# Optimization experiments

Hardware: AMD Instinct MI355X
Metric: run time of the kernel (lower is better)

Reference implementation:

```python
import jax, jax.numpy as jnp
import numpy as np

N_NODES = 100000


def _segment_mean(h, src, dst, n_nodes):
    # copy_u: gather source features along edges, then mean-reduce per dst node
    msg = h[src]                                             # [E, D]
    s = jax.ops.segment_sum(msg, dst, num_segments=n_nodes)  # [N, D]
    cnt = jax.ops.segment_sum(jnp.ones((src.shape[0],), h.dtype), dst,
                              num_segments=n_nodes)          # [N]
    return s / jnp.maximum(cnt, 1.0)[:, None]


def setup_inputs() -> dict:
    key = jax.random.key(0)
    k1, k2, k3, k4, k5 = jax.random.split(key, 5)
    in_feats, n_hidden, n_classes = 128, 128, 64
    n_edges = 1600000
    features = jax.random.normal(k1, (N_NODES, in_feats), dtype=jnp.float32)
    W1 = jax.random.normal(k2, (in_feats, n_hidden), dtype=jnp.float32) * (1.0 / np.sqrt(in_feats))
    b1 = jnp.zeros((n_hidden,), jnp.float32)
    W2 = jax.random.normal(k3, (n_hidden, n_classes), dtype=jnp.float32) * (1.0 / np.sqrt(n_hidden))
    b2 = jnp.zeros((n_classes,), jnp.float32)
    src = jax.random.randint(k4, (n_edges,), 0, N_NODES, dtype=jnp.int64)
    dst = jax.random.randint(k5, (n_edges,), 0, N_NODES, dtype=jnp.int64)
    return {"features": features, "W1": W1, "b1": b1, "W2": W2, "b2": b2,
            "src": src, "dst": dst}


def reference(features, W1, b1, W2, b2, src, dst):
    # Layer 0: mean aggregation -> Linear -> relu  (dropout p=0.0 is identity)
    h = _segment_mean(features, src, dst, N_NODES)
    h = jax.nn.relu(h @ W1 + b1)
    # Layer 1: mean aggregation -> Linear (no activation on output layer)
    h = _segment_mean(h, src, dst, N_NODES)
    h = h @ W2 + b2
    return h
```

## Files before the change

kernel.cpp:

```cpp
#include <hip/hip_runtime.h>

#define N_NODES 100000
#define D 128
#define NE 1600000
#define C_OUT 64
#define NB 391
#define SENT 100000
#define P2B 320
#define P2E 5000
#define SEGSTRIDE 5120

typedef _Float16 half8 __attribute__((ext_vector_type(8)));
typedef float floatx4 __attribute__((ext_vector_type(4)));


__device__ inline half8 shfl_xor_h8(half8 v, int mask) {
    union { half8 h; int i[4]; } u;
    u.h = v;
    u.i[0] = __shfl_xor(u.i[0], mask);
    u.i[1] = __shfl_xor(u.i[1], mask);
    u.i[2] = __shfl_xor(u.i[2], mask);
    u.i[3] = __shfl_xor(u.i[3], mask);
    return u.h;
}

__device__ inline void pack_one(const float* W, _Float16* Wp, int tid, int N) {
    int l = tid & 63, p = tid >> 6;
    int nt = p >> 2, kc = p & 3;
    int quad = l >> 4, c = l & 15;
    int n = nt * 16 + c;
    half8 h;
    #pragma unroll
    for (int j = 0; j < 8; ++j) {
        int k = kc * 32 + quad * 8 + j;
        h[j] = (_Float16)W[k * N + n];
    }
    *(half8*)(Wp + (size_t)p * 512 + l * 8) = h;
}

__global__ __launch_bounds__(256) void setup_kernel(const float* __restrict__ W1,
                                                    const float* __restrict__ W2,
                                                    _Float16* __restrict__ wp1,
                                                    _Float16* __restrict__ wp2,
                                                    int* __restrict__ t1s,
                                                    int* __restrict__ t2s) {
    const int blk = blockIdx.x;
    const int t = threadIdx.x;
    if (blk < 8) {
        pack_one(W1, wp1, blk * 256 + t, 128);
    } else if (blk < 12) {
        pack_one(W2, wp2, (blk - 8) * 256 + t, 64);
    } else {
        if (t < 64) t1s[t] = 0;
        else if (t < 96) t2s[t - 64] = 0;
    }
}

__global__ __launch_bounds__(1024) void p2_part(const int* __restrict__ src,
                                                const int* __restrict__ dst,
                                                unsigned* __restrict__ gwords,
                                                int* __restrict__ ofsg) {
    __shared__ unsigned ebuf[P2E];
    __shared__ int hist[NB];
    __shared__ int ofs[NB + 1];
    __shared__ int cur[NB];
    __shared__ int sc[512];
    const int t = threadIdx.x;
    const int base = blockIdx.x * P2E;

    for (int i = t; i < NB; i += 1024) hist[i] = 0;
    __syncthreads();

    unsigned w[5];
    int bk[5];
    #pragma unroll
    for (int r = 0; r < 5; ++r) {
        const int e = base + r * 1024 + t;
        if (r * 1024 + t < P2E) {
            const int d = dst[e];
            w[r] = ((unsigned)(d & 255) << 20) | (unsigned)src[e];
            bk[r] = d >> 8;
            atomicAdd(&hist[bk[r]], 1);
        } else {
            bk[r] = -1;
        }
    }
    __syncthreads();

    if (t < 512) sc[t] = (t < NB) ? hist[t] : 0;
    __syncthreads();
    for (int off = 1; off < 512; off <<= 1) {
        int y = 0;
        if (t < 512 && t >= off) y = sc[t - off];
        __syncthreads();
        if (t < 512) sc[t] += y;
        __syncthreads();
    }
    if (t < NB) {
        const int ex = sc[t] - hist[t];
        ofs[t] = ex;
        cur[t] = ex;
    }
    if (t == 0) ofs[NB] = P2E;
    __syncthreads();

    #pragma unroll
    for (int r = 0; r < 5; ++r) {
        if (bk[r] >= 0) {
            const int slot = atomicAdd(&cur[bk[r]], 1);
            ebuf[slot] = w[r];
        }
    }
    __syncthreads();

    unsigned* gout = gwords + (size_t)blockIdx.x * SEGSTRIDE;
    for (int i = t; i < P2E; i += 1024) gout[i] = ebuf[i];
    int* oout = ofsg + blockIdx.x * (NB + 1);
    for (int i = t; i < NB + 1; i += 1024) oout[i] = ofs[i];
}

__global__ __launch_bounds__(512) void p_scan2(const int* __restrict__ ofsg,
                                               int* __restrict__ bbase) {
    __shared__ int lds[512];
    const int t = threadIdx.x;
    int tot = 0;
    if (t < NB) {
        for (int blk = 0; blk < P2B; ++blk) {
            const int* row = ofsg + blk * (NB + 1);
            tot += row[t + 1] - row[t];
        }
    }
    lds[t] = tot;
    __syncthreads();
    for (int off = 1; off < 512; off <<= 1) {
        int y = (t >= off) ? lds[t - off] : 0;
        __syncthreads();
        lds[t] += y;
        __syncthreads();
    }
    if (t < NB) bbase[t] = lds[t] - tot;
    if (t == 0) bbase[NB] = NE;
}

__global__ __launch_bounds__(256) void p3_finalize(const unsigned* __restrict__ gwords,
                                                   const int* __restrict__ ofsg,
                                                   const int* __restrict__ bbase,
                                                   int* __restrict__ ptrp,
                                                   int* __restrict__ pcnt,
                                                   float* __restrict__ inv,
                                                   int* __restrict__ csr) {
    __shared__ unsigned wbuf[8192];
    __shared__ int lcnt[256];
    __shared__ int lofs[256];
    __shared__ int cursor;
    const int b = blockIdx.x;
    const int t = threadIdx.x;
    if (t == 0) cursor = 0;
    lcnt[t] = 0;
    __syncthreads();

    for (int blk = t; blk < P2B; blk += 256) {
        const int* row = ofsg + blk * (NB + 1);
        const int a = row[b];
        const int len = row[b + 1] - a;
        if (len > 0) {
            const int o = atomicAdd(&cursor, len);
            if (o + len <= 8192) {
                const unsigned* s = gwords + (size_t)blk * SEGSTRIDE + a;
                for (int j = 0; j < len; ++j) {
                    const unsigned w = s[j];
                    wbuf[o + j] = w;
                    atomicAdd(&lcnt[(w >> 20) & 255], 1);
                }
            }
        }
    }
    __syncthreads();

    const int tot = cursor;
    const int v = lcnt[t];
    const int pc = (v + 7) & ~7;
    lofs[t] = pc;
    __syncthreads();
    for (int off = 1; off < 256; off <<= 1) {
        int y = (t >= off) ? lofs[t - off] : 0;
        __syncthreads();
        lofs[t] += y;
        __syncthreads();
    }
    const int ex = lofs[t] - pc;
    const int pad_base = bbase[b] + 1792 * b;

    const int node = b * 256 + t;
    if (node < N_NODES) {
        ptrp[node] = pad_base + ex;
        pcnt[node] = pc;
        inv[node] = 1.0f / fmaxf((float)v, 1.0f);
    }
    for (int j = v; j < pc; ++j) csr[pad_base + ex + j] = SENT;

    __syncthreads();
    lofs[t] = ex;
    __syncthreads();
    for (int i = t; i < tot; i += 256) {
        const unsigned w = wbuf[i];
        const int pos = atomicAdd(&lofs[(w >> 20) & 255], 1);
        csr[pad_base + pos] = (int)(w & 0xFFFFF);
    }
}

__global__ __launch_bounds__(256) void gemm1(const float* __restrict__ A,
                                             const _Float16* __restrict__ Wp,
                                             _Float16* __restrict__ outh) {
    __shared__ __align__(16) _Float16 Wl[16384];
    __shared__ __align__(16) _Float16 Al[4096];
    const int t = threadIdx.x;
    {
        const floatx4* s4 = (const floatx4*)Wp;
        floatx4* d4 = (floatx4*)Wl;
        #pragma unroll
        for (int i = 0; i < 8; ++i) d4[t + 256 * i] = s4[t + 256 * i];
    }
    const int lane = t & 63;
    const int wave = t >> 6;
    const int row0 = blockIdx.x * 128;

    floatx4 acc[8][2];
    #pragma unroll
    for (int mt = 0; mt < 8; ++mt)
        #pragma unroll
        for (int nt = 0; nt < 2; ++nt) acc[mt][nt] = (floatx4)0.0f;

    for (int kc = 0; kc < 4; ++kc) {
        __syncthreads();
        #pragma unroll
        for (int rep = 0; rep < 2; ++rep) {
            int p = rep * 256 + t;
            int r = p >> 2, quad = p & 3;
            int row = row0 + r;
            if (row > N_NODES - 1) row = N_NODES - 1;
            const float4 x0 = *(const float4*)(A + (size_t)row * D + kc * 32 + quad * 8);
            const float4 x1 = *(const float4*)(A + (size_t)row * D + kc * 32 + quad * 8 + 4);
            half8 h;
            h[0] = (_Float16)x0.x; h[1] = (_Float16)x0.y;
            h[2] = (_Float16)x0.z; h[3] = (_Float16)x0.w;
            h[4] = (_Float16)x1.x; h[5] = (_Float16)x1.y;
            h[6] = (_Float16)x1.z; h[7] = (_Float16)x1.w;
            int mt = r >> 4, m = r & 15;
            *(half8*)(Al + mt * 512 + (quad * 16 + m) * 8) = h;
        }
        __syncthreads();
        const half8* Af = (const half8*)Al;
        const half8* Bf = (const half8*)Wl;
        half8 b0 = Bf[((wave * 2 + 0) * 4 + kc) * 64 + lane];
        half8 b1 = Bf[((wave * 2 + 1) * 4 + kc) * 64 + lane];
        #pragma unroll
        for (int mt = 0; mt < 8; ++mt) {
            half8 a = Af[mt * 64 + lane];
            acc[mt][0] = __builtin_amdgcn_mfma_f32_16x16x32_f16(a, b0, acc[mt][0], 0, 0, 0);
            acc[mt][1] = __builtin_amdgcn_mfma_f32_16x16x32_f16(a, b1, acc[mt][1], 0, 0, 0);
        }
    }

    const int quad = lane >> 4, cl = lane & 15;
    #pragma unroll
    for (int mt = 0; mt < 8; ++mt)
        #pragma unroll
        for (int nt = 0; nt < 2; ++nt) {
            int col = wave * 32 + nt * 16 + cl;
            #pragma unroll
            for (int i = 0; i < 4; ++i) {
                int row = row0 + mt * 16 + quad * 4 + i;
                if (row < N_NODES)
                    outh[(size_t)row * D + col] = (_Float16)acc[mt][nt][i];
            }
        }
}

__global__ __launch_bounds__(256) void gemm2(const _Float16* __restrict__ Ah,
                                             const _Float16* __restrict__ Wp,
                                             _Float16* __restrict__ outh) {
    __shared__ __align__(16) _Float16 Wl[8192];
    __shared__ __align__(16) _Float16 Al[4096];
    const int t = threadIdx.x;
    {
        const floatx4* s4 = (const floatx4*)Wp;
        floatx4* d4 = (floatx4*)Wl;
        #pragma unroll
        for (int i = 0; i < 4; ++i) d4[t + 256 * i] = s4[t + 256 * i];
    }
    const int lane = t & 63;
    const int wave = t >> 6;
    const int row0 = blockIdx.x * 128;

    floatx4 acc[8];
    #pragma unroll
    for (int mt = 0; mt < 8; ++mt) acc[mt] = (floatx4)0.0f;

    for (int kc = 0; kc < 4; ++kc) {
        __syncthreads();
        #pragma unroll
        for (int rep = 0; rep < 2; ++rep) {
            int p = rep * 256 + t;
            int r = p >> 2, quad = p & 3;
            int row = row0 + r;
            if (row > N_NODES - 1) row = N_NODES - 1;
            half8 h = *(const half8*)(Ah + (size_t)row * D + kc * 32 + quad * 8);
            int mt = r >> 4, m = r & 15;
            *(half8*)(Al + mt * 512 + (quad * 16 + m) * 8) = h;
        }
        __syncthreads();
        const half8* Af = (const half8*)Al;
        const half8* Bf = (const half8*)Wl;
        half8 b = Bf[(wave * 4 + kc) * 64 + lane];
        #pragma unroll
        for (int mt = 0; mt < 8; ++mt) {
            half8 a = Af[mt * 64 + lane];
            acc[mt] = __builtin_amdgcn_mfma_f32_16x16x32_f16(a, b, acc[mt], 0, 0, 0);
        }
    }

    const int quad = lane >> 4, cl = lane & 15;
    const int col = wave * 16 + cl;
    #pragma unroll
    for (int mt = 0; mt < 8; ++mt)
        #pragma unroll
        for (int i = 0; i < 4; ++i) {
            int row = row0 + mt * 16 + quad * 4 + i;
            if (row < N_NODES)
                outh[(size_t)row * C_OUT + col] = (_Float16)acc[mt][i];
        }
}

__global__ __launch_bounds__(256) void agg128h(const _Float16* __restrict__ f,
                                               const int* __restrict__ ptrp,
                                               const int* __restrict__ pcnt,
                                               const int* __restrict__ csr,
                                               const float* __restrict__ inv,
                                               const float* __restrict__ bias,
                                               _Float16* __restrict__ outh) {
    const int wave = threadIdx.x >> 6;
    const int lane = threadIdx.x & 63;
    const int q = lane & 15, hf = lane >> 4;
    const int n = blockIdx.x * 4 + wave;
    const int begin = ptrp[n];
    const int end = begin + pcnt[n];
    const half8* f8 = (const half8*)f;

    half8 acc0 = {0, 0, 0, 0, 0, 0, 0, 0};
    half8 acc1 = {0, 0, 0, 0, 0, 0, 0, 0};
    for (int base = begin; base < end; base += 64) {
        const int m = min(64, end - base);
        int edge = (lane < m) ? csr[base + lane] : SENT;
        for (int i = 0; i < m; i += 8) {
            int s0 = __shfl(edge, i + hf);
            int s1 = __shfl(edge, i + 4 + hf);
            half8 v0 = f8[(size_t)s0 * 16 + q];
            half8 v1 = f8[(size_t)s1 * 16 + q];
            acc0 += v0;
            acc1 += v1;
        }
    }
    acc0 += acc1;
    acc0 += shfl_xor_h8(acc0, 16);
    acc0 += shfl_xor_h8(acc0, 32);
    if (hf == 0) {
        const float iv = inv[n];
        const float4 b0 = ((const float4*)bias)[q * 2];
        const float4 b1 = ((const float4*)bias)[q * 2 + 1];
        half8 o;
        o[0] = (_Float16)fmaxf((float)acc0[0] * iv + b0.x, 0.f);
        o[1] = (_Float16)fmaxf((float)acc0[1] * iv + b0.y, 0.f);
        o[2] = (_Float16)fmaxf((float)acc0[2] * iv + b0.z, 0.f);
        o[3] = (_Float16)fmaxf((float)acc0[3] * iv + b0.w, 0.f);
        o[4] = (_Float16)fmaxf((float)acc0[4] * iv + b1.x, 0.f);
        o[5] = (_Float16)fmaxf((float)acc0[5] * iv + b1.y, 0.f);
        o[6] = (_Float16)fmaxf((float)acc0[6] * iv + b1.z, 0.f);
        o[7] = (_Float16)fmaxf((float)acc0[7] * iv + b1.w, 0.f);
        ((half8*)outh)[(size_t)n * 16 + q] = o;
    }
}

__global__ __launch_bounds__(256) void agg64h(const _Float16* __restrict__ f,
                                              const int* __restrict__ ptrp,
                                              const int* __restrict__ pcnt,
                                              const int* __restrict__ csr,
                                              const float* __restrict__ inv,
                                              const float* __restrict__ bias,
                                              float* __restrict__ out) {
    const int wave = threadIdx.x >> 6;
    const int lane = threadIdx.x & 63;
    const int q = lane & 7, hf = lane >> 3;
    const int n = blockIdx.x * 4 + wave;
    const int begin = ptrp[n];
    const int end = begin + pcnt[n];
    const half8* f8 = (const half8*)f;

    half8 acc0 = {0, 0, 0, 0, 0, 0, 0, 0};
    half8 acc1 = {0, 0, 0, 0, 0, 0, 0, 0};
    for (int base = begin; base < end; base += 64) {
        const int m = min(64, end - base);
        int edge = (lane < m) ? csr[base + lane] : SENT;
        int i = 0;
        for (; i + 16 <= m; i += 16) {
            int s0 = __shfl(edge, i + hf);
            int s1 = __shfl(edge, i + 8 + hf);
            half8 v0 = f8[(size_t)s0 * 8 + q];
            half8 v1 = f8[(size_t)s1 * 8 + q];
            acc0 += v0;
            acc1 += v1;
        }
        if (i < m) {
            int s = __shfl(edge, i + hf);
            acc0 += f8[(size_t)s * 8 + q];
        }
    }
    acc0 += acc1;
    acc0 += shfl_xor_h8(acc0, 8);
    acc0 += shfl_xor_h8(acc0, 16);
    acc0 += shfl_xor_h8(acc0, 32);
    if (hf == 0) {
        const float iv = inv[n];
        const float4 b0 = ((const float4*)bias)[q * 2];
        const float4 b1 = ((const float4*)bias)[q * 2 + 1];
        float4 o0, o1;
        o0.x = (float)acc0[0] * iv + b0.x;
        o0.y = (float)acc0[1] * iv + b0.y;
        o0.z = (float)acc0[2] * iv + b0.z;
        o0.w = (float)acc0[3] * iv + b0.w;
        o1.x = (float)acc0[4] * iv + b1.x;
        o1.y = (float)acc0[5] * iv + b1.y;
        o1.z = (float)acc0[6] * iv + b1.z;
        o1.w = (float)acc0[7] * iv + b1.w;
        ((float4*)out)[(size_t)n * 16 + q * 2] = o0;
        ((float4*)out)[(size_t)n * 16 + q * 2 + 1] = o1;
    }
}

extern "C" void kernel_launch(void* const* d_in, const int* in_sizes, int n_in,
                              void* d_out, int out_size, void* d_ws, size_t ws_size,
                              hipStream_t stream) {
    const float* features = (const float*)d_in[0];
    const float* W1 = (const float*)d_in[1];
    const float* b1 = (const float*)d_in[2];
    const float* W2 = (const float*)d_in[3];
    const float* b2 = (const float*)d_in[4];
    const int* src = (const int*)d_in[5];
    const int* dst = (const int*)d_in[6];
    float* out = (float*)d_out;

    char* ws = (char*)d_ws;
    int*      bbase = (int*)(ws + 0L * 4);
    int*      ofsg  = (int*)(ws + 512L * 4);
    int*      ptrp  = (int*)(ws + 125952L * 4);
    int*      pcnt  = (int*)(ws + 225952L * 4);
    float*    inv   = (float*)(ws + 325952L * 4);
    int*      csr   = (int*)(ws + 425952L * 4);
    unsigned* gwords= (unsigned*)(ws + 2825952L * 4);
    _Float16* wp1   = (_Float16*)(ws + 4464352L * 4);
    _Float16* wp2   = (_Float16*)(ws + 4472544L * 4);
    _Float16* t1h   = (_Float16*)(ws + 4476640L * 4);
    _Float16* h1h   = (_Float16*)(ws + 10876704L * 4);
    _Float16* t2h   = (_Float16*)(ws + 17276704L * 4);

    setup_kernel<<<13, 256, 0, stream>>>(W1, W2, wp1, wp2,
                                         (int*)(t1h + (size_t)SENT * 128),
                                         (int*)(t2h + (size_t)SENT * 64));
    p2_part<<<P2B, 1024, 0, stream>>>(src, dst, gwords, ofsg);
    p_scan2<<<1, 512, 0, stream>>>(ofsg, bbase);
    p3_finalize<<<NB, 256, 0, stream>>>(gwords, ofsg, bbase, ptrp, pcnt, inv, csr);

    const int gemm_grid = (N_NODES + 127) / 128;

    gemm1<<<gemm_grid, 256, 0, stream>>>(features, wp1, t1h);
    agg128h<<<N_NODES / 4, 256, 0, stream>>>(t1h, ptrp, pcnt, csr, inv, b1, h1h);

    gemm2<<<gemm_grid, 256, 0, stream>>>(h1h, wp2, t2h);
    agg64h<<<N_NODES / 4, 256, 0, stream>>>(t2h, ptrp, pcnt, csr, inv, b2, out);
}
```

Measured before the change: 272.7 us.

## Parallelize bucket-total scan, use wave-shuffle scans, deepen aggregation unrolling

Several changes at once. The single-block serial reduction over partition rows is split into a per-bucket parallel sum kernel followed by a small scan kernel. The LDS Hillis-Steele scans in the partition and finalize kernels are replaced with wave shuffle scans plus per-wave totals. The partition block count drops to 256 with more edges per block. Both aggregation kernels unroll the gather loop to four loads in flight and hoist the inv load out of the epilogue. These target the serial scan bottleneck and gather latency, at the cost of one extra kernel launch and higher register pressure.

```diff
diff --git a/kernel.cpp b/kernel.cpp
--- a/kernel.cpp
+++ b/kernel.cpp
@@ -6,9 +6,9 @@
 #define C_OUT 64
 #define NB 391
 #define SENT 100000
-#define P2B 320
-#define P2E 5000
-#define SEGSTRIDE 5120
+#define P2B 256
+#define P2E 6250
+#define SEGSTRIDE 6400
 
 typedef _Float16 half8 __attribute__((ext_vector_type(8)));
 typedef float floatx4 __attribute__((ext_vector_type(4)));
@@ -64,19 +64,20 @@
     __shared__ int hist[NB];
     __shared__ int ofs[NB + 1];
     __shared__ int cur[NB];
-    __shared__ int sc[512];
+    __shared__ int wsum[8];
     const int t = threadIdx.x;
     const int base = blockIdx.x * P2E;
 
     for (int i = t; i < NB; i += 1024) hist[i] = 0;
     __syncthreads();
 
-    unsigned w[5];
-    int bk[5];
-    #pragma unroll
-    for (int r = 0; r < 5; ++r) {
-        const int e = base + r * 1024 + t;
-        if (r * 1024 + t < P2E) {
+    unsigned w[7];
+    int bk[7];
+    #pragma unroll
+    for (int r = 0; r < 7; ++r) {
+        const int j = r * 1024 + t;
+        if (j < P2E) {
+            const int e = base + j;
             const int d = dst[e];
             w[r] = ((unsigned)(d & 255) << 20) | (unsigned)src[e];
             bk[r] = d >> 8;
@@ -87,17 +88,19 @@
     }
     __syncthreads();
 
-    if (t < 512) sc[t] = (t < NB) ? hist[t] : 0;
-    __syncthreads();
-    for (int off = 1; off < 512; off <<= 1) {
-        int y = 0;
-        if (t < 512 && t >= off) y = sc[t - off];
-        __syncthreads();
-        if (t < 512) sc[t] += y;
-        __syncthreads();
-    }
+    int v = 0, incl = 0;
+    if (t < 512) { v = (t < NB) ? hist[t] : 0; incl = v; }
+    #pragma unroll
+    for (int d = 1; d < 64; d <<= 1) {
+        int y = __shfl_up(incl, d);
+        if ((t & 63) >= d) incl += y;
+    }
+    if (t < 512 && (t & 63) == 63) wsum[t >> 6] = incl;
+    __syncthreads();
     if (t < NB) {
-        const int ex = sc[t] - hist[t];
+        int ex = incl - v;
+        const int wv = t >> 6;
+        for (int j = 0; j < wv; ++j) ex += wsum[j];
         ofs[t] = ex;
         cur[t] = ex;
     }
@@ -105,7 +108,7 @@
     __syncthreads();
 
     #pragma unroll
-    for (int r = 0; r < 5; ++r) {
+    for (int r = 0; r < 7; ++r) {
         if (bk[r] >= 0) {
             const int slot = atomicAdd(&cur[bk[r]], 1);
             ebuf[slot] = w[r];
@@ -119,26 +122,37 @@
     for (int i = t; i < NB + 1; i += 1024) oout[i] = ofs[i];
 }
 
-__global__ __launch_bounds__(512) void p_scan2(const int* __restrict__ ofsg,
+__global__ __launch_bounds__(256) void p_sum(const int* __restrict__ ofsg,
+                                             int* __restrict__ btot) {
+    __shared__ int ws4[4];
+    const int b = blockIdx.x;
+    const int t = threadIdx.x;
+    const int* row = ofsg + t * (NB + 1);
+    int d = row[b + 1] - row[b];
+    #pragma unroll
+    for (int m = 1; m < 64; m <<= 1) d += __shfl_xor(d, m);
+    if ((t & 63) == 0) ws4[t >> 6] = d;
+    __syncthreads();
+    if (t == 0) btot[b] = ws4[0] + ws4[1] + ws4[2] + ws4[3];
+}
+
+__global__ __launch_bounds__(512) void p_scanB(const int* __restrict__ btot,
                                                int* __restrict__ bbase) {
-    __shared__ int lds[512];
-    const int t = threadIdx.x;
-    int tot = 0;
-    if (t < NB) {
-        for (int blk = 0; blk < P2B; ++blk) {
-            const int* row = ofsg + blk * (NB + 1);
-            tot += row[t + 1] - row[t];
-        }
-    }
-    lds[t] = tot;
-    __syncthreads();
-    for (int off = 1; off < 512; off <<= 1) {
-        int y = (t >= off) ? lds[t - off] : 0;
-        __syncthreads();
-        lds[t] += y;
-        __syncthreads();
-    }
-    if (t < NB) bbase[t] = lds[t] - tot;
+    __shared__ int wsum[8];
+    const int t = threadIdx.x;
+    int v = (t < NB) ? btot[t] : 0;
+    int incl = v;
+    #pragma unroll
+    for (int d = 1; d < 64; d <<= 1) {
+        int y = __shfl_up(incl, d);
+        if ((t & 63) >= d) incl += y;
+    }
+    if ((t & 63) == 63) wsum[t >> 6] = incl;
+    __syncthreads();
+    int ex = incl - v;
+    const int wv = t >> 6;
+    for (int j = 0; j < wv; ++j) ex += wsum[j];
+    if (t < NB) bbase[t] = ex;
     if (t == 0) bbase[NB] = NE;
 }
 
@@ -152,6 +166,7 @@
     __shared__ unsigned wbuf[8192];
     __shared__ int lcnt[256];
     __shared__ int lofs[256];
+    __shared__ int ws4[4];
     __shared__ int cursor;
     const int b = blockIdx.x;
     const int t = threadIdx.x;
@@ -180,15 +195,19 @@
     const int tot = cursor;
     const int v = lcnt[t];
     const int pc = (v + 7) & ~7;
-    lofs[t] = pc;
-    __syncthreads();
-    for (int off = 1; off < 256; off <<= 1) {
-        int y = (t >= off) ? lofs[t - off] : 0;
-        __syncthreads();
-        lofs[t] += y;
-        __syncthreads();
-    }
-    const int ex = lofs[t] - pc;
+    int incl = pc;
+    #pragma unroll
+    for (int d = 1; d < 64; d <<= 1) {
+        int y = __shfl_up(incl, d);
+        if ((t & 63) >= d) incl += y;
+    }
+    if ((t & 63) == 63) ws4[t >> 6] = incl;
+    __syncthreads();
+    int ex = incl - pc;
+    {
+        const int wv = t >> 6;
+        for (int j = 0; j < wv; ++j) ex += ws4[j];
+    }
     const int pad_base = bbase[b] + 1792 * b;
 
     const int node = b * 256 + t;
@@ -345,6 +364,7 @@
     const int n = blockIdx.x * 4 + wave;
     const int begin = ptrp[n];
     const int end = begin + pcnt[n];
+    const float iv = inv[n];
     const half8* f8 = (const half8*)f;
 
     half8 acc0 = {0, 0, 0, 0, 0, 0, 0, 0};
@@ -352,7 +372,22 @@
     for (int base = begin; base < end; base += 64) {
         const int m = min(64, end - base);
         int edge = (lane < m) ? csr[base + lane] : SENT;
-        for (int i = 0; i < m; i += 8) {
+        int i = 0;
+        for (; i + 16 <= m; i += 16) {
+            int s0 = __shfl(edge, i + hf);
+            int s1 = __shfl(edge, i + 4 + hf);
+            int s2 = __shfl(edge, i + 8 + hf);
+            int s3 = __shfl(edge, i + 12 + hf);
+            half8 v0 = f8[(size_t)s0 * 16 + q];
+            half8 v1 = f8[(size_t)s1 * 16 + q];
+            half8 v2 = f8[(size_t)s2 * 16 + q];
+            half8 v3 = f8[(size_t)s3 * 16 + q];
+            acc0 += v0;
+            acc1 += v1;
+            acc0 += v2;
+            acc1 += v3;
+        }
+        if (i < m) {
             int s0 = __shfl(edge, i + hf);
             int s1 = __shfl(edge, i + 4 + hf);
             half8 v0 = f8[(size_t)s0 * 16 + q];
@@ -365,7 +400,6 @@
     acc0 += shfl_xor_h8(acc0, 16);
     acc0 += shfl_xor_h8(acc0, 32);
     if (hf == 0) {
-        const float iv = inv[n];
         const float4 b0 = ((const float4*)bias)[q * 2];
         const float4 b1 = ((const float4*)bias)[q * 2 + 1];
         half8 o;
@@ -394,6 +428,7 @@
     const int n = blockIdx.x * 4 + wave;
     const int begin = ptrp[n];
     const int end = begin + pcnt[n];
+    const float iv = inv[n];
     const half8* f8 = (const half8*)f;
 
     half8 acc0 = {0, 0, 0, 0, 0, 0, 0, 0};
@@ -402,13 +437,28 @@
         const int m = min(64, end - base);
         int edge = (lane < m) ? csr[base + lane] : SENT;
         int i = 0;
-        for (; i + 16 <= m; i += 16) {
+        for (; i + 32 <= m; i += 32) {
+            int s0 = __shfl(edge, i + hf);
+            int s1 = __shfl(edge, i + 8 + hf);
+            int s2 = __shfl(edge, i + 16 + hf);
+            int s3 = __shfl(edge, i + 24 + hf);
+            half8 v0 = f8[(size_t)s0 * 8 + q];
+            half8 v1 = f8[(size_t)s1 * 8 + q];
+            half8 v2 = f8[(size_t)s2 * 8 + q];
+            half8 v3 = f8[(size_t)s3 * 8 + q];
+            acc0 += v0;
+            acc1 += v1;
+            acc0 += v2;
+            acc1 += v3;
+        }
+        if (i + 16 <= m) {
             int s0 = __shfl(edge, i + hf);
             int s1 = __shfl(edge, i + 8 + hf);
             half8 v0 = f8[(size_t)s0 * 8 + q];
             half8 v1 = f8[(size_t)s1 * 8 + q];
             acc0 += v0;
             acc1 += v1;
+            i += 16;
         }
         if (i < m) {
             int s = __shfl(edge, i + hf);
@@ -420,7 +470,6 @@
     acc0 += shfl_xor_h8(acc0, 16);
     acc0 += shfl_xor_h8(acc0, 32);
     if (hf == 0) {
-        const float iv = inv[n];
         const float4 b0 = ((const float4*)bias)[q * 2];
         const float4 b1 = ((const float4*)bias)[q * 2 + 1];
         float4 o0, o1;
@@ -452,6 +501,7 @@
     char* ws = (char*)d_ws;
     int*      bbase = (int*)(ws + 0L * 4);
     int*      ofsg  = (int*)(ws + 512L * 4);
+    int*      btot  = (int*)(ws + 100864L * 4);
     int*      ptrp  = (int*)(ws + 125952L * 4);
     int*      pcnt  = (int*)(ws + 225952L * 4);
     float*    inv   = (float*)(ws + 325952L * 4);
@@ -467,7 +517,8 @@
                                          (int*)(t1h + (size_t)SENT * 128),
                                          (int*)(t2h + (size_t)SENT * 64));
     p2_part<<<P2B, 1024, 0, stream>>>(src, dst, gwords, ofsg);
-    p_scan2<<<1, 512, 0, stream>>>(ofsg, bbase);
+    p_sum<<<NB, 256, 0, stream>>>(ofsg, btot);
+    p_scanB<<<1, 512, 0, stream>>>(btot, bbase);
     p3_finalize<<<NB, 256, 0, stream>>>(gwords, ofsg, bbase, ptrp, pcnt, inv, csr);
 
     const int gemm_grid = (N_NODES + 127) / 128;
```

After: 250.2 us. 1.09x faster.
